# Optimization experiments

Hardware: AMD Instinct MI355X
Metric: run time of the kernel (lower is better)

## Reference

```python
import jax, jax.numpy as jnp
import numpy as np

SIZE_SEQ = 2048
DK = 64

def setup_inputs() -> dict:
    key = jax.random.key(0)
    k1, k2, k3, k4 = jax.random.split(key, 4)
    Q = jax.random.normal(k1, (8, 4096, DK), jnp.float32)
    K = jax.random.normal(k2, (8, 4096, DK), jnp.float32)
    V = jax.random.normal(k3, (8, 4096, DK), jnp.float32)
    stdv = 1.0 / np.sqrt(DK)  # initmat_ uses dim=0 -> size dk
    Krelpos = jax.random.uniform(k4, (DK, SIZE_SEQ), jnp.float32, -stdv, stdv)
    return {"Q": Q, "K": K, "V": V, "Krelpos": Krelpos}

def reference(Q, K, V, Krelpos):
    N, S, dk = Q.shape
    ss = SIZE_SEQ
    b = N * (S // ss)  # S is a multiple of sizeSeq, so prepare() is a pure reshape
    Qb = Q.reshape(b, ss, dk)
    Kb = K.reshape(b, ss, dk)
    Vb = V.reshape(b, ss, dk)
    # QK^T scores
    QK = jnp.einsum('bsd,btd->bst', Qb, Kb)
    # relative-position bias via skew trick: pad a zero column, reshape (ss, ss+1)->(ss+1, ss), drop first row
    QP = jnp.einsum('bsd,dt->bst', Qb, Krelpos)
    z = jnp.zeros((b, ss, 1), Qb.dtype)
    QP = jnp.concatenate([z, QP], axis=2).reshape(b, ss + 1, ss)[:, 1:, :]
    QK = QK + QP
    # causal mask: -inf above the diagonal
    mask = jnp.triu(jnp.full((ss, ss), -jnp.inf, dtype=Qb.dtype), k=1)
    A = jax.nn.softmax(QK / jnp.sqrt(jnp.asarray(dk, Qb.dtype)) + mask, axis=2)
    out = jnp.einsum('bst,btd->bsd', A, Vb)
    return out.reshape(N, S, dk)
```

## Files before the change

### kernel.cpp

```cpp
#include <hip/hip_runtime.h>
#include <hip/hip_bf16.h>

#define SS 2048
#define DK 64
#define NB 16

typedef unsigned short u16;
typedef u16   u16x8 __attribute__((ext_vector_type(8)));
typedef u16   u16x4 __attribute__((ext_vector_type(4)));
typedef short s16x8 __attribute__((ext_vector_type(8)));
typedef float f32x16 __attribute__((ext_vector_type(16)));
typedef unsigned u32x4 __attribute__((ext_vector_type(4)));

__device__ __forceinline__ u16 f2bf(float f) {
    unsigned u = __builtin_bit_cast(unsigned, f);
    return (u16)((u + 0x7fffu + ((u >> 16) & 1u)) >> 16);
}
__device__ __forceinline__ float bf2f(u16 v) {
    unsigned u = ((unsigned)v) << 16;
    return __builtin_bit_cast(float, u);
}
__device__ __forceinline__ unsigned cvtpk(float lo, float hi) {
    unsigned d;
    asm("v_cvt_pk_bf16_f32 %0, %1, %2" : "=v"(d) : "v"(lo), "v"(hi));
    return d;
}
__device__ __forceinline__ f32x16 zero16() {
    f32x16 z;
    #pragma unroll
    for (int i = 0; i < 16; ++i) z[i] = 0.f;
    return z;
}

__launch_bounds__(256)
__global__ void prep_kernel(const float* __restrict__ K,
                            const float* __restrict__ V,
                            const float* __restrict__ R,
                            u16* __restrict__ Kb,
                            u16* __restrict__ VTb,
                            u16* __restrict__ RTb) {
    __shared__ float tl[64][65];
    const int bid = blockIdx.x, tid = threadIdx.x;

    if (bid < 2048) {
        size_t i0 = ((size_t)bid * 256 + tid) * 4;
        float4 v = *(const float4*)(K + i0);
        u16x4 o;
        o[0] = f2bf(v.x); o[1] = f2bf(v.y); o[2] = f2bf(v.z); o[3] = f2bf(v.w);
        *(u16x4*)(Kb + i0) = o;
    } else if (bid < 2560) {
        int u = bid - 2048;
        int bb = u >> 5, t0 = (u & 31) * 64;
        #pragma unroll
        for (int p = 0; p < 4; ++p) {
            int tt = (tid >> 4) + p * 16;
            int d0 = (tid & 15) * 4;
            float4 v = *(const float4*)(V + ((size_t)(bb * SS + t0 + tt)) * DK + d0);
            tl[tt][d0 + 0] = v.x; tl[tt][d0 + 1] = v.y;
            tl[tt][d0 + 2] = v.z; tl[tt][d0 + 3] = v.w;
        }
        __syncthreads();
        int d = tid >> 2, q = tid & 3;
        #pragma unroll
        for (int v2 = 0; v2 < 8; ++v2) {
            int t = q * 16 + 2 * v2;
            unsigned dw = ((unsigned)f2bf(tl[t + 1][d]) << 16) | f2bf(tl[t][d]);
            *(unsigned*)(VTb + ((size_t)(bb * DK + d)) * SS + t0 + t) = dw;
        }
    } else {
        int u = bid - 2560;
        int c0 = u * 64;
        #pragma unroll
        for (int p = 0; p < 4; ++p) {
            int dd = (tid >> 4) + p * 16;
            int cc0 = (tid & 15) * 4;
            float4 v = *(const float4*)(R + (size_t)dd * SS + c0 + cc0);
            tl[dd][cc0 + 0] = v.x; tl[dd][cc0 + 1] = v.y;
            tl[dd][cc0 + 2] = v.z; tl[dd][cc0 + 3] = v.w;
        }
        __syncthreads();
        int cc = tid >> 2, q = tid & 3;
        #pragma unroll
        for (int v2 = 0; v2 < 8; ++v2) {
            int d = q * 16 + 2 * v2;
            unsigned dw = ((unsigned)f2bf(tl[d + 1][cc]) << 16) | f2bf(tl[d][cc]);
            *(unsigned*)(RTb + ((size_t)(c0 + cc)) * DK + d) = dw;
        }
    }
}

__launch_bounds__(256, 1)
__global__ void attn_mfma(const float* __restrict__ Q,
                          const u16* __restrict__ Kb,
                          const u16* __restrict__ VTb,
                          const u16* __restrict__ RTb,
                          float* __restrict__ O) {
    __shared__ alignas(16) u16 VTl[2][64 * 128];
    __shared__ alignas(16) u16 QPl[4][32 * 64];

    const int tid  = threadIdx.x;
    const int b    = blockIdx.y;
    const int x    = blockIdx.x;
    const int jjb  = ((x >> 1) + (b & 7) * 2) & 15;
    const int flip = (x & 1) ^ ((b >> 3) & 1);
    const int jj   = flip ? (31 - jjb) : jjb;
    const int S0   = jj * 64;
    const int wave = tid >> 6, lane = tid & 63;
    const int h    = lane >> 5, sl = lane & 31;
    const int grp  = wave >> 1, wv = wave & 1;
    const int s0w  = S0 + wv * 32;
    const int rtb  = wv ? 0 : 32;
    const int nTt  = (jj >> 1) + 1;
    const int itMax = (nTt + 1) >> 1;
    unsigned* QPwU = (unsigned*)&QPl[wave][0];

    s16x8 bq[4];
    {
        const float* Qr = Q + (size_t)(b * SS + s0w + sl) * DK;
        #pragma unroll
        for (int k = 0; k < 4; ++k) {
            float4 a = *(const float4*)(Qr + 16 * k + 8 * h);
            float4 c = *(const float4*)(Qr + 16 * k + 8 * h + 4);
            u16x8 t;
            t[0] = f2bf(a.x * 0.125f); t[1] = f2bf(a.y * 0.125f);
            t[2] = f2bf(a.z * 0.125f); t[3] = f2bf(a.w * 0.125f);
            t[4] = f2bf(c.x * 0.125f); t[5] = f2bf(c.y * 0.125f);
            t[6] = f2bf(c.z * 0.125f); t[7] = f2bf(c.w * 0.125f);
            bq[k] = __builtin_bit_cast(s16x8, t);
        }
    }

    f32x16 o0 = zero16(), o1 = zero16();
    float m = -3e38f, l = 0.f;

    auto qpfrag = [&](int mi, int cbase) {
        f32x16 acc = zero16();
        int c = cbase + rtb + mi * 32 + sl;
        c = max(0, min(2047, c));
        const u16* Rp = RTb + (size_t)c * DK + 8 * h;
        #pragma unroll
        for (int k = 0; k < 4; ++k) {
            s16x8 a = *(const s16x8*)(Rp + 16 * k);
            acc = __builtin_amdgcn_mfma_f32_32x32x16_bf16(a, bq[k], acc, 0, 0, 0);
        }
        #pragma unroll
        for (int R = 0; R < 4; ++R)
            #pragma unroll
            for (int rp = 0; rp < 2; ++rp) {
                int crel = mi * 32 + 8 * R + 2 * rp + 4 * h;
                unsigned dw = cvtpk(acc[4 * R + 2 * rp], acc[4 * R + 2 * rp + 1]);
                int col = (crel + 2 * sl) & 63;
                QPwU[sl * 32 + (col >> 1)] = dw;
            }
    };
    auto biasmask = [&](f32x16& s, int ti, int t0, bool fullv) {
        #pragma unroll
        for (int r = 0; r < 16; ++r) {
            int off = (r & 3) + 8 * (r >> 2);
            int col = (31 + ti * 32 + off + 4 * h + sl) & 63;
            unsigned dv = QPwU[sl * 32 + (col >> 1)];
            float bias = bf2f((u16)(dv >> ((col & 1) * 16)));
            float v = s[r] + bias;
            if (!fullv) {
                int t = t0 + ti * 32 + off + 4 * h;
                v = (t <= s0w + sl) ? v : -3e38f;
            }
            s[r] = v;
        }
    };

    for (int it = 0; it < itMax; ++it) {
        const int tl = 2 * it + grp;
        const bool active = (tl < nTt);
        const int t0 = tl * 128;

        if (active) {
            int gtid = tid & 127;
            #pragma unroll
            for (int i = 0; i < 8; ++i) {
                int ch = gtid + i * 128;
                int d = ch >> 4, co = ch & 15;
                u16x8 v = *(const u16x8*)(VTb + (size_t)(b * DK + d) * SS + t0 + co * 8);
                *(u16x8*)((char*)&VTl[grp][0] + d * 256 + ((co * 16) ^ ((d & 7) << 4))) = v;
            }
        }
        __syncthreads();

        if (active) {
            const int cbase = 1984 + t0 - S0;
            s16x8 kf[4][4];
            {
                const u16* Kp = Kb + (size_t)(b * SS + t0 + sl) * DK + 8 * h;
                #pragma unroll
                for (int ti = 0; ti < 4; ++ti)
                    #pragma unroll
                    for (int k = 0; k < 4; ++k)
                        kf[ti][k] = *(const s16x8*)(Kp + ti * 32 * DK + 16 * k);
            }
            auto qk = [&](int ti) -> f32x16 {
                f32x16 acc = zero16();
                #pragma unroll
                for (int k = 0; k < 4; ++k)
                    acc = __builtin_amdgcn_mfma_f32_32x32x16_bf16(kf[ti][k], bq[k], acc, 0, 0, 0);
                return acc;
            };

            const bool fullv = (t0 + 127 <= s0w);
            qpfrag(0, cbase); qpfrag(1, cbase);
            f32x16 s0v = qk(0); biasmask(s0v, 0, t0, fullv);
            qpfrag(2, cbase);
            f32x16 s1v = qk(1); biasmask(s1v, 1, t0, fullv);
            qpfrag(3, cbase);
            f32x16 s2v = qk(2); biasmask(s2v, 2, t0, fullv);
            qpfrag(4, cbase);
            f32x16 s3v = qk(3); biasmask(s3v, 3, t0, fullv);

            float tmax = -3e38f;
            #pragma unroll
            for (int r = 0; r < 16; ++r) {
                tmax = fmaxf(tmax, s0v[r]); tmax = fmaxf(tmax, s1v[r]);
                tmax = fmaxf(tmax, s2v[r]); tmax = fmaxf(tmax, s3v[r]);
            }
            tmax = fmaxf(tmax, __shfl_xor(tmax, 32));
            float mn = fmaxf(m, tmax);
            float corr = __expf(m - mn);
            m = mn;
            float ps = 0.f;
            #pragma unroll
            for (int r = 0; r < 16; ++r) {
                s0v[r] = __expf(s0v[r] - mn); ps += s0v[r];
                s1v[r] = __expf(s1v[r] - mn); ps += s1v[r];
                s2v[r] = __expf(s2v[r] - mn); ps += s2v[r];
                s3v[r] = __expf(s3v[r] - mn); ps += s3v[r];
            }
            l = l * corr + ps;
            #pragma unroll
            for (int r = 0; r < 16; ++r) { o0[r] *= corr; o1[r] *= corr; }

            unsigned pd[4][4][2];
            #define PACK_P(TI, SV)                                            \
                _Pragma("unroll")                                             \
                for (int R = 0; R < 4; ++R) {                                 \
                    pd[TI][R][0] = cvtpk(SV[4 * R + 0], SV[4 * R + 1]);       \
                    pd[TI][R][1] = cvtpk(SV[4 * R + 2], SV[4 * R + 3]);       \
                }
            PACK_P(0, s0v) PACK_P(1, s1v) PACK_P(2, s2v) PACK_P(3, s3v)
            #undef PACK_P

            #pragma unroll
            for (int c = 0; c < 8; ++c) {
                const int ti = c >> 1;
                const int R0 = (2 * c) & 3, R1 = (2 * c + 1) & 3;
                unsigned a0 = pd[ti][R0][0], a1 = pd[ti][R0][1];
                unsigned b0 = pd[ti][R1][0], b1 = pd[ti][R1][1];
                unsigned xa0 = __shfl_xor(a0, 32), xa1 = __shfl_xor(a1, 32);
                unsigned xb0 = __shfl_xor(b0, 32), xb1 = __shfl_xor(b1, 32);
                u32x4 pw;
                pw[0] = h ? xb0 : a0;
                pw[1] = h ? xb1 : a1;
                pw[2] = h ? b0 : xa0;
                pw[3] = h ? b1 : xa1;
                s16x8 pb = __builtin_bit_cast(s16x8, pw);
                s16x8 va0 = *(const s16x8*)((const char*)&VTl[grp][0] + (0 * 32 + sl) * 256 +
                                            ((32 * c + 16 * h) ^ ((sl & 7) << 4)));
                s16x8 va1 = *(const s16x8*)((const char*)&VTl[grp][0] + (1 * 32 + sl) * 256 +
                                            ((32 * c + 16 * h) ^ ((sl & 7) << 4)));
                o0 = __builtin_amdgcn_mfma_f32_32x32x16_bf16(va0, pb, o0, 0, 0, 0);
                o1 = __builtin_amdgcn_mfma_f32_32x32x16_bf16(va1, pb, o1, 0, 0, 0);
            }
        }
        __syncthreads();
    }

    float* scr = (float*)&VTl[0][0];
    if (grp == 1) {
        int base = (wv * 64 + lane) * 34;
        scr[base + 0] = m;
        scr[base + 1] = l;
        #pragma unroll
        for (int j = 0; j < 16; ++j) { scr[base + 2 + j] = o0[j]; scr[base + 18 + j] = o1[j]; }
    }
    __syncthreads();
    if (grp == 0) {
        int base = (wv * 64 + lane) * 34;
        float mB = scr[base + 0], lB = scr[base + 1];
        float M  = fmaxf(m, mB);
        float fa = __expf(m - M), fb = __expf(mB - M);
        float lt = l * fa + lB * fb;
        #pragma unroll
        for (int j = 0; j < 16; ++j) {
            o0[j] = o0[j] * fa + scr[base + 2 + j] * fb;
            o1[j] = o1[j] * fa + scr[base + 18 + j] * fb;
        }
        lt = lt + __shfl_xor(lt, 32);
        float inv = 1.0f / lt;
        float* Or = O + (size_t)(b * SS + s0w + sl) * DK;
        #pragma unroll
        for (int R = 0; R < 4; ++R) {
            float4 w;
            w.x = o0[4 * R + 0] * inv; w.y = o0[4 * R + 1] * inv;
            w.z = o0[4 * R + 2] * inv; w.w = o0[4 * R + 3] * inv;
            *(float4*)(Or + 8 * R + 4 * h) = w;
            w.x = o1[4 * R + 0] * inv; w.y = o1[4 * R + 1] * inv;
            w.z = o1[4 * R + 2] * inv; w.w = o1[4 * R + 3] * inv;
            *(float4*)(Or + 32 + 8 * R + 4 * h) = w;
        }
    }
}

#define RT_ 64
#define TT_ 64
#define NWAVES_ 4
#define PATCH_C_ 128
#define PATCH_STRIDE_ 72

struct MrgT {
    float macc[RT_][DK + 1];
    float mw[NWAVES_][RT_];
    float lw[NWAVES_][RT_];
    float linv[RT_];
};
union SMemT {
    u16 patch[NWAVES_][PATCH_C_ * PATCH_STRIDE_];
    MrgT mrg;
};

__launch_bounds__(256)
__global__ void attn_relpos_fallback(const float* __restrict__ Q,
                                     const float* __restrict__ K,
                                     const float* __restrict__ V,
                                     const float* __restrict__ R,
                                     float* __restrict__ O) {
    __shared__ __attribute__((aligned(16))) SMemT sm;
    const int tileIdx = blockIdx.x;
    const int b       = blockIdx.y;
    const int r0      = tileIdx * RT_;
    const int wave    = __builtin_amdgcn_readfirstlane((int)(threadIdx.x >> 6));
    const int lane    = (int)(threadIdx.x & 63);
    const int s       = r0 + lane;

    float q[DK];
    {
        const float4* Qp = reinterpret_cast<const float4*>(Q + (size_t)(b * SS + s) * DK);
        #pragma unroll
        for (int i = 0; i < DK / 4; ++i) {
            float4 v = Qp[i];
            q[4*i+0] = v.x; q[4*i+1] = v.y; q[4*i+2] = v.z; q[4*i+3] = v.w;
        }
    }
    float acc[DK];
    #pragma unroll
    for (int d = 0; d < DK; ++d) acc[d] = 0.f;
    float m = -1e30f, l = 0.f;
    const int numT = r0 / TT_ + 1;

    for (int ti = wave; ti < numT; ti += NWAVES_) {
        const int t0 = ti * TT_;
        const int c0 = (SS - RT_) + t0 - r0;
        #pragma unroll
        for (int i = 0; i < 32; ++i) {
            const int d  = (lane >> 5) + 2 * i;
            const int cb = (lane & 31) * 4;
            const int c  = c0 + cb;
            float4 v = make_float4(0.f, 0.f, 0.f, 0.f);
            if (c < SS) v = *reinterpret_cast<const float4*>(R + (size_t)d * SS + c);
            u16* pw = &sm.patch[wave][0];
            pw[(cb + 0) * PATCH_STRIDE_ + d] = f2bf(v.x);
            pw[(cb + 1) * PATCH_STRIDE_ + d] = f2bf(v.y);
            pw[(cb + 2) * PATCH_STRIDE_ + d] = f2bf(v.z);
            pw[(cb + 3) * PATCH_STRIDE_ + d] = f2bf(v.w);
        }
        asm volatile("s_waitcnt lgkmcnt(0)" ::: "memory");
        const int ttlim = min(TT_ - 1, (r0 - t0) + lane);
        for (int tc = 0; tc < TT_; tc += 16) {
            float sc[16];
            #pragma unroll
            for (int j = 0; j < 16; ++j) {
                const int tt = tc + j;
                const int t  = t0 + tt;
                const float4* Kt4 = reinterpret_cast<const float4*>(K + (size_t)(b * SS + t) * DK);
                float a0 = 0.f, a1 = 0.f, a2 = 0.f, a3 = 0.f;
                #pragma unroll
                for (int i = 0; i < 16; ++i) {
                    float4 kv = Kt4[i];
                    a0 = fmaf(q[4*i+0], kv.x, a0);
                    a1 = fmaf(q[4*i+1], kv.y, a1);
                    a2 = fmaf(q[4*i+2], kv.z, a2);
                    a3 = fmaf(q[4*i+3], kv.w, a3);
                }
                const int cc = (RT_ - 1) + tt - lane;
                const u16* rp = &sm.patch[wave][cc * PATCH_STRIDE_];
                #pragma unroll
                for (int i = 0; i < 8; ++i) {
                    u16x8 v8 = *reinterpret_cast<const u16x8*>(rp + 8 * i);
                    a0 = fmaf(q[8*i+0], bf2f(v8[0]), a0);
                    a1 = fmaf(q[8*i+1], bf2f(v8[1]), a1);
                    a2 = fmaf(q[8*i+2], bf2f(v8[2]), a2);
                    a3 = fmaf(q[8*i+3], bf2f(v8[3]), a3);
                    a0 = fmaf(q[8*i+4], bf2f(v8[4]), a0);
                    a1 = fmaf(q[8*i+5], bf2f(v8[5]), a1);
                    a2 = fmaf(q[8*i+6], bf2f(v8[6]), a2);
                    a3 = fmaf(q[8*i+7], bf2f(v8[7]), a3);
                }
                const float v = ((a0 + a1) + (a2 + a3)) * 0.125f;
                sc[j] = (tt <= ttlim) ? v : -1e30f;
            }
            float cm = sc[0];
            #pragma unroll
            for (int j = 1; j < 16; ++j) cm = fmaxf(cm, sc[j]);
            const float nm   = fmaxf(m, cm);
            const float corr = __expf(m - nm);
            m = nm; l *= corr;
            #pragma unroll
            for (int d = 0; d < DK; ++d) acc[d] *= corr;
            #pragma unroll
            for (int j = 0; j < 16; ++j) {
                const int t = t0 + tc + j;
                const float p = __expf(sc[j] - m);
                l += p;
                const float4* Vt4 = reinterpret_cast<const float4*>(V + (size_t)(b * SS + t) * DK);
                #pragma unroll
                for (int i = 0; i < 16; ++i) {
                    float4 vv = Vt4[i];
                    acc[4*i+0] = fmaf(p, vv.x, acc[4*i+0]);
                    acc[4*i+1] = fmaf(p, vv.y, acc[4*i+1]);
                    acc[4*i+2] = fmaf(p, vv.z, acc[4*i+2]);
                    acc[4*i+3] = fmaf(p, vv.w, acc[4*i+3]);
                }
            }
        }
    }
    __syncthreads();
    sm.mrg.mw[wave][lane] = m;
    sm.mrg.lw[wave][lane] = l;
    __syncthreads();
    float M = sm.mrg.mw[0][lane];
    #pragma unroll
    for (int w = 1; w < NWAVES_; ++w) M = fmaxf(M, sm.mrg.mw[w][lane]);
    float L = 0.f;
    #pragma unroll
    for (int w = 0; w < NWAVES_; ++w) L += sm.mrg.lw[w][lane] * __expf(sm.mrg.mw[w][lane] - M);
    const float myscale = __expf(m - M);
    for (int w = 0; w < NWAVES_; ++w) {
        if (wave == w) {
            if (w == 0) {
                #pragma unroll
                for (int d = 0; d < DK; ++d) sm.mrg.macc[lane][d] = acc[d] * myscale;
            } else {
                #pragma unroll
                for (int d = 0; d < DK; ++d) sm.mrg.macc[lane][d] += acc[d] * myscale;
            }
        }
        __syncthreads();
    }
    if (wave == 0) sm.mrg.linv[lane] = 1.0f / L;
    __syncthreads();
    const int row = (int)(threadIdx.x >> 2);
    const int dq  = (int)(threadIdx.x & 3) * 16;
    const float li = sm.mrg.linv[row];
    float4* Orow = reinterpret_cast<float4*>(O + (size_t)(b * SS + r0 + row) * DK + dq);
    #pragma unroll
    for (int k2 = 0; k2 < 4; ++k2) {
        float4 o;
        o.x = sm.mrg.macc[row][dq + 4*k2 + 0] * li;
        o.y = sm.mrg.macc[row][dq + 4*k2 + 1] * li;
        o.z = sm.mrg.macc[row][dq + 4*k2 + 2] * li;
        o.w = sm.mrg.macc[row][dq + 4*k2 + 3] * li;
        Orow[k2] = o;
    }
}

extern "C" void kernel_launch(void* const* d_in, const int* in_sizes, int n_in,
                              void* d_out, int out_size, void* d_ws, size_t ws_size,
                              hipStream_t stream) {
    (void)in_sizes; (void)n_in; (void)out_size;
    const float* Q = (const float*)d_in[0];
    const float* K = (const float*)d_in[1];
    const float* V = (const float*)d_in[2];
    const float* R = (const float*)d_in[3];
    float* O = (float*)d_out;

    const size_t KB_ELEMS = (size_t)NB * SS * DK;
    const size_t RT_ELEMS = (size_t)SS * DK;
    const size_t NEED = (2 * KB_ELEMS + RT_ELEMS) * sizeof(u16);

    if (ws_size >= NEED) {
        u16* Kb  = (u16*)d_ws;
        u16* VTb = Kb + KB_ELEMS;
        u16* RTb = VTb + KB_ELEMS;
        prep_kernel<<<2592, 256, 0, stream>>>(K, V, R, Kb, VTb, RTb);
        attn_mfma<<<dim3(32, 16), 256, 0, stream>>>(Q, Kb, VTb, RTb, O);
    } else {
        attn_relpos_fallback<<<dim3(SS / RT_, NB), 256, 0, stream>>>(Q, K, V, R, O);
    }
}
```

Baseline: 101.3 us.

## Process key tile in 32-row sub-tiles with per-subtile online softmax

Splits each 128-key tile into four 32-key sub-tiles, loading K fragments, computing scores, updating the running max/sum, and accumulating P·V per sub-tile. This cuts live registers for K fragments and score accumulators, which may help occupancy or avoid spills. In exchange it quadruples the output rescaling and max/shuffle reductions, and it serializes the score-to-PV dependency with less batched load latency hiding.

```diff
diff --git a/kernel.cpp b/kernel.cpp
--- a/kernel.cpp
+++ b/kernel.cpp
@@ -188,85 +188,68 @@
 
         if (active) {
             const int cbase = 1984 + t0 - S0;
-            s16x8 kf[4][4];
-            {
-                const u16* Kp = Kb + (size_t)(b * SS + t0 + sl) * DK + 8 * h;
-                #pragma unroll
-                for (int ti = 0; ti < 4; ++ti)
+            const bool fullv = (t0 + 127 <= s0w);
+
+            qpfrag(0, cbase);
+            #pragma unroll
+            for (int ti = 0; ti < 4; ++ti) {
+                s16x8 kf[4];
+                {
+                    const u16* Kp = Kb + (size_t)(b * SS + t0 + ti * 32 + sl) * DK + 8 * h;
                     #pragma unroll
                     for (int k = 0; k < 4; ++k)
-                        kf[ti][k] = *(const s16x8*)(Kp + ti * 32 * DK + 16 * k);
-            }
-            auto qk = [&](int ti) -> f32x16 {
-                f32x16 acc = zero16();
+                        kf[k] = *(const s16x8*)(Kp + 16 * k);
+                }
+                qpfrag(ti + 1, cbase);
+
+                f32x16 s = zero16();
                 #pragma unroll
                 for (int k = 0; k < 4; ++k)
-                    acc = __builtin_amdgcn_mfma_f32_32x32x16_bf16(kf[ti][k], bq[k], acc, 0, 0, 0);
-                return acc;
-            };
-
-            const bool fullv = (t0 + 127 <= s0w);
-            qpfrag(0, cbase); qpfrag(1, cbase);
-            f32x16 s0v = qk(0); biasmask(s0v, 0, t0, fullv);
-            qpfrag(2, cbase);
-            f32x16 s1v = qk(1); biasmask(s1v, 1, t0, fullv);
-            qpfrag(3, cbase);
-            f32x16 s2v = qk(2); biasmask(s2v, 2, t0, fullv);
-            qpfrag(4, cbase);
-            f32x16 s3v = qk(3); biasmask(s3v, 3, t0, fullv);
-
-            float tmax = -3e38f;
-            #pragma unroll
-            for (int r = 0; r < 16; ++r) {
-                tmax = fmaxf(tmax, s0v[r]); tmax = fmaxf(tmax, s1v[r]);
-                tmax = fmaxf(tmax, s2v[r]); tmax = fmaxf(tmax, s3v[r]);
-            }
-            tmax = fmaxf(tmax, __shfl_xor(tmax, 32));
-            float mn = fmaxf(m, tmax);
-            float corr = __expf(m - mn);
-            m = mn;
-            float ps = 0.f;
-            #pragma unroll
-            for (int r = 0; r < 16; ++r) {
-                s0v[r] = __expf(s0v[r] - mn); ps += s0v[r];
-                s1v[r] = __expf(s1v[r] - mn); ps += s1v[r];
-                s2v[r] = __expf(s2v[r] - mn); ps += s2v[r];
-                s3v[r] = __expf(s3v[r] - mn); ps += s3v[r];
-            }
-            l = l * corr + ps;
-            #pragma unroll
-            for (int r = 0; r < 16; ++r) { o0[r] *= corr; o1[r] *= corr; }
-
-            unsigned pd[4][4][2];
-            #define PACK_P(TI, SV)                                            \
-                _Pragma("unroll")                                             \
-                for (int R = 0; R < 4; ++R) {                                 \
-                    pd[TI][R][0] = cvtpk(SV[4 * R + 0], SV[4 * R + 1]);       \
-                    pd[TI][R][1] = cvtpk(SV[4 * R + 2], SV[4 * R + 3]);       \
-                }
-            PACK_P(0, s0v) PACK_P(1, s1v) PACK_P(2, s2v) PACK_P(3, s3v)
-            #undef PACK_P
-
-            #pragma unroll
-            for (int c = 0; c < 8; ++c) {
-                const int ti = c >> 1;
-                const int R0 = (2 * c) & 3, R1 = (2 * c + 1) & 3;
-                unsigned a0 = pd[ti][R0][0], a1 = pd[ti][R0][1];
-                unsigned b0 = pd[ti][R1][0], b1 = pd[ti][R1][1];
-                unsigned xa0 = __shfl_xor(a0, 32), xa1 = __shfl_xor(a1, 32);
-                unsigned xb0 = __shfl_xor(b0, 32), xb1 = __shfl_xor(b1, 32);
-                u32x4 pw;
-                pw[0] = h ? xb0 : a0;
-                pw[1] = h ? xb1 : a1;
-                pw[2] = h ? b0 : xa0;
-                pw[3] = h ? b1 : xa1;
-                s16x8 pb = __builtin_bit_cast(s16x8, pw);
-                s16x8 va0 = *(const s16x8*)((const char*)&VTl[grp][0] + (0 * 32 + sl) * 256 +
-                                            ((32 * c + 16 * h) ^ ((sl & 7) << 4)));
-                s16x8 va1 = *(const s16x8*)((const char*)&VTl[grp][0] + (1 * 32 + sl) * 256 +
-                                            ((32 * c + 16 * h) ^ ((sl & 7) << 4)));
-                o0 = __builtin_amdgcn_mfma_f32_32x32x16_bf16(va0, pb, o0, 0, 0, 0);
-                o1 = __builtin_amdgcn_mfma_f32_32x32x16_bf16(va1, pb, o1, 0, 0, 0);
+                    s = __builtin_amdgcn_mfma_f32_32x32x16_bf16(kf[k], bq[k], s, 0, 0, 0);
+                biasmask(s, ti, t0, fullv);
+
+                float tmax = -3e38f;
+                #pragma unroll
+                for (int r = 0; r < 16; ++r) tmax = fmaxf(tmax, s[r]);
+                tmax = fmaxf(tmax, __shfl_xor(tmax, 32));
+                float mn = fmaxf(m, tmax);
+                float corr = __expf(m - mn);
+                m = mn;
+                float ps = 0.f;
+                #pragma unroll
+                for (int r = 0; r < 16; ++r) { s[r] = __expf(s[r] - mn); ps += s[r]; }
+                l = l * corr + ps;
+                #pragma unroll
+                for (int r = 0; r < 16; ++r) { o0[r] *= corr; o1[r] *= corr; }
+
+                unsigned pd[4][2];
+                #pragma unroll
+                for (int R = 0; R < 4; ++R) {
+                    pd[R][0] = cvtpk(s[4 * R + 0], s[4 * R + 1]);
+                    pd[R][1] = cvtpk(s[4 * R + 2], s[4 * R + 3]);
+                }
+
+                #pragma unroll
+                for (int c2 = 0; c2 < 2; ++c2) {
+                    const int c = 2 * ti + c2;
+                    const int R0 = 2 * c2, R1 = 2 * c2 + 1;
+                    unsigned a0 = pd[R0][0], a1 = pd[R0][1];
+                    unsigned b0 = pd[R1][0], b1 = pd[R1][1];
+                    unsigned xa0 = __shfl_xor(a0, 32), xa1 = __shfl_xor(a1, 32);
+                    unsigned xb0 = __shfl_xor(b0, 32), xb1 = __shfl_xor(b1, 32);
+                    u32x4 pw;
+                    pw[0] = h ? xb0 : a0;
+                    pw[1] = h ? xb1 : a1;
+                    pw[2] = h ? b0 : xa0;
+                    pw[3] = h ? b1 : xa1;
+                    s16x8 pb = __builtin_bit_cast(s16x8, pw);
+                    s16x8 va0 = *(const s16x8*)((const char*)&VTl[grp][0] + (0 * 32 + sl) * 256 +
+                                                ((32 * c + 16 * h) ^ ((sl & 7) << 4)));
+                    s16x8 va1 = *(const s16x8*)((const char*)&VTl[grp][0] + (1 * 32 + sl) * 256 +
+                                                ((32 * c + 16 * h) ^ ((sl & 7) << 4)));
+                    o0 = __builtin_amdgcn_mfma_f32_32x32x16_bf16(va0, pb, o0, 0, 0, 0);
+                    o1 = __builtin_amdgcn_mfma_f32_32x32x16_bf16(va1, pb, o1, 0, 0, 0);
+                }
             }
         }
         __syncthreads();
```

Result: slower. 124.3 us (+22.8%).
